# Kernel tuning notes

Hardware: AMD Instinct MI355X
Metric: run time of the kernel (lower is better)

The kernel has to match this reference:

```python
import jax, jax.numpy as jnp
import numpy as np

MOMENTUM = 0.05
EPS = 1e-06


def _gated_ema(x, g):
    """y[t] = (1 - g[t]) * y[t-1] + g[t] * x[t], y[-1] = 0.
    x: (B, C, T), g: (B, 1, T) -> (B, C, T)"""
    xT = jnp.moveaxis(x, -1, 0)  # (T, B, C)
    gT = jnp.moveaxis(g, -1, 0)  # (T, B, 1)
    init = jnp.zeros(x.shape[:-1], x.dtype)  # (B, C)

    def step(carry, inp):
        xt, gt = inp
        carry = (1.0 - gt) * carry + gt * xt
        return carry, carry

    _, ys = jax.lax.scan(step, init, (xT, gT))
    return jnp.moveaxis(ys, 0, -1)


def setup_inputs() -> dict:
    key = jax.random.key(0)
    ks = jax.random.split(key, 6)
    B, C, T = 8, 512, 8192
    return {
        "x": jax.random.normal(ks[0], (B, C, T), dtype=jnp.float32),
        "g": jax.random.uniform(ks[1], (B, 1, T), dtype=jnp.float32),
        "Wa_w": jax.random.normal(ks[2], (1, C, 1), dtype=jnp.float32),
        "Wb_w": jax.random.normal(ks[3], (1, C, 1), dtype=jnp.float32),
        "Wo_w": jax.random.normal(ks[4], (C, 1, 1), dtype=jnp.float32),
        "Wo_b": jax.random.normal(ks[5], (C,), dtype=jnp.float32),
    }


def reference(x, g, Wa_w, Wb_w, Wo_w, Wo_b):
    sg = jax.lax.stop_gradient
    C = x.shape[1]
    g = g * MOMENTUM  # time-varying momentum gate
    # Wa: 1x1 conv C->1 with softmax over input channels (convex combination)
    wa = jax.nn.softmax(Wa_w, axis=1)  # (1, C, 1)
    mean = jnp.sum(wa * _gated_ema(sg(x), g), axis=1, keepdims=True)  # (B, 1, T)
    xc = x - mean
    wb = jax.nn.softmax(Wb_w, axis=1)  # (1, C, 1)
    var = jnp.sum(wb * _gated_ema(jnp.square(sg(xc)), g), axis=1, keepdims=True)  # (B, 1, T)
    xn = xc / jnp.sqrt(var + EPS)
    # Wo: grouped 1x1 conv (groups=C) == per-channel scale + bias
    return xn * Wo_w.reshape(1, C, 1) + Wo_b.reshape(1, C, 1)
```

## Files before the change

kernel.cpp:

```cpp
#include <hip/hip_runtime.h>

constexpr int BB = 8, CC = 512, TT = 8192;
static_assert((TT & (TT - 1)) == 0 && (CC & (CC - 1)) == 0, "pow2");
constexpr int LOG_T = 13, LOG_C = 9;
constexpr float MOM = 0.05f, EPSV = 1e-6f;

typedef float v4f __attribute__((ext_vector_type(4)));

__global__ __launch_bounds__(256) void k_reduce_c(const float* __restrict__ x,
                                                  const float* __restrict__ Wa,
                                                  const float* __restrict__ Wb,
                                                  float* __restrict__ sa,
                                                  float* __restrict__ sb,
                                                  float* __restrict__ sb2) {
  __shared__ float lwa[CC];
  __shared__ float lwb[CC];
  __shared__ float xw[8];
  __shared__ float red[3][4][256];
  const int tid = threadIdx.x;
  const int lane = tid & 63;
  const int wid = tid >> 6;

  float va0 = Wa[tid], va1 = Wa[tid + 256];
  float vb0 = Wb[tid], vb1 = Wb[tid + 256];
  float ma = fmaxf(va0, va1), mb = fmaxf(vb0, vb1);
  #pragma unroll
  for (int off = 32; off > 0; off >>= 1) {
    ma = fmaxf(ma, __shfl_down(ma, off, 64));
    mb = fmaxf(mb, __shfl_down(mb, off, 64));
  }
  if (lane == 0) { xw[wid] = ma; xw[4 + wid] = mb; }
  __syncthreads();
  ma = fmaxf(fmaxf(xw[0], xw[1]), fmaxf(xw[2], xw[3]));
  mb = fmaxf(fmaxf(xw[4], xw[5]), fmaxf(xw[6], xw[7]));
  float ea0 = expf(va0 - ma), ea1 = expf(va1 - ma);
  float eb0 = expf(vb0 - mb), eb1 = expf(vb1 - mb);
  float sA = ea0 + ea1, sB = eb0 + eb1;
  #pragma unroll
  for (int off = 32; off > 0; off >>= 1) {
    sA += __shfl_down(sA, off, 64);
    sB += __shfl_down(sB, off, 64);
  }
  __syncthreads();
  if (lane == 0) { xw[wid] = sA; xw[4 + wid] = sB; }
  __syncthreads();
  sA = xw[0] + xw[1] + xw[2] + xw[3];
  sB = xw[4] + xw[5] + xw[6] + xw[7];
  const float rA = 1.f / sA, rB = 1.f / sB;
  lwa[tid] = ea0 * rA; lwa[tid + 256] = ea1 * rA;
  lwb[tid] = eb0 * rB; lwb[tid + 256] = eb1 * rB;
  __syncthreads();

  const int tilesPerB = TT / 256;
  const int b = blockIdx.x / tilesPerB;
  const int tbase = (blockIdx.x % tilesPerB) * 256;
  const int t = tbase + lane * 4;
  const float* xp = x + ((size_t)(b * CC + wid * 128)) * TT + t;

  float a0=0,a1=0,a2=0,a3=0;
  float b0=0,b1=0,b2=0,b3=0;
  float q0=0,q1=0,q2=0,q3=0;
  const int cbase = wid * 128;
  #pragma unroll 4
  for (int cc = 0; cc < 128; ++cc) {
    float4 xv = *(const float4*)(xp + (size_t)cc * TT);
    float wac = lwa[cbase + cc];
    float wbc = lwb[cbase + cc];
    a0 = fmaf(wac, xv.x, a0); a1 = fmaf(wac, xv.y, a1);
    a2 = fmaf(wac, xv.z, a2); a3 = fmaf(wac, xv.w, a3);
    b0 = fmaf(wbc, xv.x, b0); b1 = fmaf(wbc, xv.y, b1);
    b2 = fmaf(wbc, xv.z, b2); b3 = fmaf(wbc, xv.w, b3);
    q0 = fmaf(wbc * xv.x, xv.x, q0); q1 = fmaf(wbc * xv.y, xv.y, q1);
    q2 = fmaf(wbc * xv.z, xv.z, q2); q3 = fmaf(wbc * xv.w, xv.w, q3);
  }
  const int li = lane * 4;
  red[0][wid][li+0]=a0; red[0][wid][li+1]=a1; red[0][wid][li+2]=a2; red[0][wid][li+3]=a3;
  red[1][wid][li+0]=b0; red[1][wid][li+1]=b1; red[1][wid][li+2]=b2; red[1][wid][li+3]=b3;
  red[2][wid][li+0]=q0; red[2][wid][li+1]=q1; red[2][wid][li+2]=q2; red[2][wid][li+3]=q3;
  __syncthreads();

  if (tid < 64) {
    const int o = tid * 4;
    float oa[4], ob[4], oq[4];
    #pragma unroll
    for (int k = 0; k < 4; ++k) {
      oa[k] = red[0][0][o+k] + red[0][1][o+k] + red[0][2][o+k] + red[0][3][o+k];
      ob[k] = red[1][0][o+k] + red[1][1][o+k] + red[1][2][o+k] + red[1][3][o+k];
      oq[k] = red[2][0][o+k] + red[2][1][o+k] + red[2][2][o+k] + red[2][3][o+k];
    }
    const size_t dst = (size_t)b * TT + tbase + o;
    *(float4*)(sa  + dst) = make_float4(oa[0], oa[1], oa[2], oa[3]);
    *(float4*)(sb  + dst) = make_float4(ob[0], ob[1], ob[2], ob[3]);
    *(float4*)(sb2 + dst) = make_float4(oq[0], oq[1], oq[2], oq[3]);
  }
}

__device__ __forceinline__ float affine_scan_prev(float A, float B, int tid,
                                                  float* wAs, float* wBs) {
  const int lane = tid & 63;
  const int wid = tid >> 6;
  #pragma unroll
  for (int off = 1; off < 64; off <<= 1) {
    float pA = __shfl_up(A, off, 64);
    float pB = __shfl_up(B, off, 64);
    if (lane >= off) { B = fmaf(A, pB, B); A *= pA; }
  }
  __syncthreads();
  if (lane == 63) { wAs[wid] = A; wBs[wid] = B; }
  __syncthreads();
  float cB = 0.f;
  for (int w = 0; w < wid; ++w) cB = fmaf(wAs[w], cB, wBs[w]);
  float leA = __shfl_up(A, 1, 64);
  float leB = __shfl_up(B, 1, 64);
  if (lane == 0) { leA = 1.f; leB = 0.f; }
  return fmaf(leA, cB, leB);
}

__global__ __launch_bounds__(256) void k_scan(const float* __restrict__ g,
                                              const float* __restrict__ sa,
                                              const float* __restrict__ sb,
                                              const float* __restrict__ sb2,
                                              float* __restrict__ mean,
                                              float* __restrict__ inv) {
  constexpr int CH = TT / 256;
  __shared__ float wAs[4], wBs[4];
  const int tid = threadIdx.x;
  const size_t base = (size_t)blockIdx.x * TT + (size_t)tid * CH;

  float gt[CH], pa[CH];

  float A = 1.f, Bv = 0.f;
  #pragma unroll
  for (int j = 0; j < CH; j += 4) {
    float gv[4]; *(float4*)gv = *(const float4*)(g + base + j);
    float sv[4]; *(float4*)sv = *(const float4*)(sa + base + j);
    #pragma unroll
    for (int k = 0; k < 4; ++k) {
      float gg = gv[k] * MOM;
      gt[j + k] = gg;
      float p = gg * sv[k];
      pa[j + k] = p;
      float a = 1.f - gg;
      A *= a;
      Bv = fmaf(a, Bv, p);
    }
  }
  float m = affine_scan_prev(A, Bv, tid, wAs, wBs);

  float A2 = 1.f, B2 = 0.f;
  #pragma unroll
  for (int j = 0; j < CH; j += 4) {
    float bv[4]; *(float4*)bv = *(const float4*)(sb  + base + j);
    float qv[4]; *(float4*)qv = *(const float4*)(sb2 + base + j);
    float m4[4];
    #pragma unroll
    for (int k = 0; k < 4; ++k) {
      float a = 1.f - gt[j + k];
      m = fmaf(a, m, pa[j + k]);
      m4[k] = m;
      float vi = fmaf(m, m, fmaf(-2.f * m, bv[k], qv[k]));
      float pv = gt[j + k] * vi;
      pa[j + k] = pv;
      A2 *= a;
      B2 = fmaf(a, B2, pv);
    }
    *(float4*)(mean + base + j) = *(float4*)m4;
  }
  float v = affine_scan_prev(A2, B2, tid, wAs, wBs);

  #pragma unroll
  for (int j = 0; j < CH; j += 4) {
    float i4[4];
    #pragma unroll
    for (int k = 0; k < 4; ++k) {
      v = fmaf(1.f - gt[j + k], v, pa[j + k]);
      i4[k] = rsqrtf(v + EPSV);
    }
    *(float4*)(inv + base + j) = *(float4*)i4;
  }
}

__global__ __launch_bounds__(256) void k_out(const float* __restrict__ x,
                                             const float* __restrict__ mean,
                                             const float* __restrict__ inv,
                                             const float* __restrict__ wo,
                                             const float* __restrict__ bo,
                                             float* __restrict__ out) {
  const size_t n4 = (size_t)BB * CC * TT / 4;
  const size_t stride = (size_t)gridDim.x * blockDim.x;
  for (size_t i = (size_t)blockIdx.x * blockDim.x + threadIdx.x; i < n4; i += stride) {
    const size_t flat = i * 4;
    const int t = (int)(flat & (TT - 1));
    const size_t rem = flat >> LOG_T;
    const int c = (int)(rem & (CC - 1));
    const int b = (int)(rem >> LOG_C);
    float4 xv = *(const float4*)(x + flat);
    const size_t mi = ((size_t)b << LOG_T) + t;
    float4 m4 = *(const float4*)(mean + mi);
    float4 i4 = *(const float4*)(inv + mi);
    const float w = wo[c], bb = bo[c];
    v4f o;
    o.x = fmaf((xv.x - m4.x) * i4.x, w, bb);
    o.y = fmaf((xv.y - m4.y) * i4.y, w, bb);
    o.z = fmaf((xv.z - m4.z) * i4.z, w, bb);
    o.w = fmaf((xv.w - m4.w) * i4.w, w, bb);
    __builtin_nontemporal_store(o, (v4f*)(out + flat));
  }
}

extern "C" void kernel_launch(void* const* d_in, const int* in_sizes, int n_in,
                              void* d_out, int out_size, void* d_ws, size_t ws_size,
                              hipStream_t stream) {
  const float* x    = (const float*)d_in[0];
  const float* g    = (const float*)d_in[1];
  const float* Wa_w = (const float*)d_in[2];
  const float* Wb_w = (const float*)d_in[3];
  const float* Wo_w = (const float*)d_in[4];
  const float* Wo_b = (const float*)d_in[5];
  float* out = (float*)d_out;

  constexpr int BT = BB * TT;
  float* ws   = (float*)d_ws;
  float* sa   = ws;
  float* sb   = sa + BT;
  float* sb2  = sb + BT;
  float* mean = sb2 + BT;
  float* inv  = mean + BT;

  k_reduce_c<<<BB * (TT / 256), 256, 0, stream>>>(x, Wa_w, Wb_w, sa, sb, sb2);
  k_scan<<<BB, 256, 0, stream>>>(g, sa, sb, sb2, mean, inv);
  k_out<<<2048, 256, 0, stream>>>(x, mean, inv, Wo_w, Wo_b, out);
}
```

Baseline: 83.13 us.

## Widen blocks in reduce and scan kernels, unroll fixed-work output kernel

The channel-reduction kernel now uses 512 threads (8 waves, 64 channels each) to get more loads in flight per time tile. The scan kernel moves to 1024 threads with 8 elements per thread and preloads all inputs up front, which shortens the serial per-thread chain; the cross-wave prefix, however, is now a loop over 16 waves. The output kernel replaces its grid-stride loop with a fixed 4-iteration unrolled body over 8192 blocks. This adds more synchronisation overhead in the scan and uses more LDS in the reduction.

Result: no change. 82.52 us (-0.7%).

```diff
diff --git a/kernel.cpp b/kernel.cpp
--- a/kernel.cpp
+++ b/kernel.cpp
@@ -7,7 +7,7 @@
 
 typedef float v4f __attribute__((ext_vector_type(4)));
 
-__global__ __launch_bounds__(256) void k_reduce_c(const float* __restrict__ x,
+__global__ __launch_bounds__(512) void k_reduce_c(const float* __restrict__ x,
                                                   const float* __restrict__ Wa,
                                                   const float* __restrict__ Wb,
                                                   float* __restrict__ sa,
@@ -15,54 +15,52 @@
                                                   float* __restrict__ sb2) {
   __shared__ float lwa[CC];
   __shared__ float lwb[CC];
-  __shared__ float xw[8];
-  __shared__ float red[3][4][256];
+  __shared__ float xw[32];
+  __shared__ float red[3][8][256];
   const int tid = threadIdx.x;
   const int lane = tid & 63;
   const int wid = tid >> 6;
 
-  float va0 = Wa[tid], va1 = Wa[tid + 256];
-  float vb0 = Wb[tid], vb1 = Wb[tid + 256];
-  float ma = fmaxf(va0, va1), mb = fmaxf(vb0, vb1);
+  float va = Wa[tid], vb = Wb[tid];
+  float ma = va, mb = vb;
   #pragma unroll
   for (int off = 32; off > 0; off >>= 1) {
     ma = fmaxf(ma, __shfl_down(ma, off, 64));
     mb = fmaxf(mb, __shfl_down(mb, off, 64));
   }
-  if (lane == 0) { xw[wid] = ma; xw[4 + wid] = mb; }
-  __syncthreads();
-  ma = fmaxf(fmaxf(xw[0], xw[1]), fmaxf(xw[2], xw[3]));
-  mb = fmaxf(fmaxf(xw[4], xw[5]), fmaxf(xw[6], xw[7]));
-  float ea0 = expf(va0 - ma), ea1 = expf(va1 - ma);
-  float eb0 = expf(vb0 - mb), eb1 = expf(vb1 - mb);
-  float sA = ea0 + ea1, sB = eb0 + eb1;
+  if (lane == 0) { xw[wid] = ma; xw[8 + wid] = mb; }
+  __syncthreads();
+  ma = xw[0]; mb = xw[8];
+  #pragma unroll
+  for (int w = 1; w < 8; ++w) { ma = fmaxf(ma, xw[w]); mb = fmaxf(mb, xw[8 + w]); }
+  float ea = expf(va - ma), eb = expf(vb - mb);
+  float sA = ea, sB = eb;
   #pragma unroll
   for (int off = 32; off > 0; off >>= 1) {
     sA += __shfl_down(sA, off, 64);
     sB += __shfl_down(sB, off, 64);
   }
-  __syncthreads();
-  if (lane == 0) { xw[wid] = sA; xw[4 + wid] = sB; }
-  __syncthreads();
-  sA = xw[0] + xw[1] + xw[2] + xw[3];
-  sB = xw[4] + xw[5] + xw[6] + xw[7];
-  const float rA = 1.f / sA, rB = 1.f / sB;
-  lwa[tid] = ea0 * rA; lwa[tid + 256] = ea1 * rA;
-  lwb[tid] = eb0 * rB; lwb[tid + 256] = eb1 * rB;
+  if (lane == 0) { xw[16 + wid] = sA; xw[24 + wid] = sB; }
+  __syncthreads();
+  sA = xw[16]; sB = xw[24];
+  #pragma unroll
+  for (int w = 1; w < 8; ++w) { sA += xw[16 + w]; sB += xw[24 + w]; }
+  lwa[tid] = ea * (1.f / sA);
+  lwb[tid] = eb * (1.f / sB);
   __syncthreads();
 
   const int tilesPerB = TT / 256;
   const int b = blockIdx.x / tilesPerB;
   const int tbase = (blockIdx.x % tilesPerB) * 256;
   const int t = tbase + lane * 4;
-  const float* xp = x + ((size_t)(b * CC + wid * 128)) * TT + t;
+  const int cbase = wid * 64;
+  const float* xp = x + ((size_t)(b * CC + cbase)) * TT + t;
 
   float a0=0,a1=0,a2=0,a3=0;
   float b0=0,b1=0,b2=0,b3=0;
   float q0=0,q1=0,q2=0,q3=0;
-  const int cbase = wid * 128;
-  #pragma unroll 4
-  for (int cc = 0; cc < 128; ++cc) {
+  #pragma unroll 8
+  for (int cc = 0; cc < 64; ++cc) {
     float4 xv = *(const float4*)(xp + (size_t)cc * TT);
     float wac = lwa[cbase + cc];
     float wbc = lwb[cbase + cc];
@@ -81,12 +79,15 @@
 
   if (tid < 64) {
     const int o = tid * 4;
-    float oa[4], ob[4], oq[4];
+    float oa[4] = {0,0,0,0}, ob[4] = {0,0,0,0}, oq[4] = {0,0,0,0};
     #pragma unroll
-    for (int k = 0; k < 4; ++k) {
-      oa[k] = red[0][0][o+k] + red[0][1][o+k] + red[0][2][o+k] + red[0][3][o+k];
-      ob[k] = red[1][0][o+k] + red[1][1][o+k] + red[1][2][o+k] + red[1][3][o+k];
-      oq[k] = red[2][0][o+k] + red[2][1][o+k] + red[2][2][o+k] + red[2][3][o+k];
+    for (int w = 0; w < 8; ++w) {
+      #pragma unroll
+      for (int k = 0; k < 4; ++k) {
+        oa[k] += red[0][w][o+k];
+        ob[k] += red[1][w][o+k];
+        oq[k] += red[2][w][o+k];
+      }
     }
     const size_t dst = (size_t)b * TT + tbase + o;
     *(float4*)(sa  + dst) = make_float4(oa[0], oa[1], oa[2], oa[3]);
@@ -116,68 +117,67 @@
   return fmaf(leA, cB, leB);
 }
 
-__global__ __launch_bounds__(256) void k_scan(const float* __restrict__ g,
-                                              const float* __restrict__ sa,
-                                              const float* __restrict__ sb,
-                                              const float* __restrict__ sb2,
-                                              float* __restrict__ mean,
-                                              float* __restrict__ inv) {
-  constexpr int CH = TT / 256;
-  __shared__ float wAs[4], wBs[4];
+__global__ __launch_bounds__(1024) void k_scan(const float* __restrict__ g,
+                                               const float* __restrict__ sa,
+                                               const float* __restrict__ sb,
+                                               const float* __restrict__ sb2,
+                                               float* __restrict__ mean,
+                                               float* __restrict__ inv) {
+  constexpr int CH = 8;
+  __shared__ float wAs[16], wBs[16];
   const int tid = threadIdx.x;
   const size_t base = (size_t)blockIdx.x * TT + (size_t)tid * CH;
 
+  float gv[CH], av[CH], bv[CH], qv[CH];
+  *(float4*)(gv)     = *(const float4*)(g   + base);
+  *(float4*)(gv + 4) = *(const float4*)(g   + base + 4);
+  *(float4*)(av)     = *(const float4*)(sa  + base);
+  *(float4*)(av + 4) = *(const float4*)(sa  + base + 4);
+  *(float4*)(bv)     = *(const float4*)(sb  + base);
+  *(float4*)(bv + 4) = *(const float4*)(sb  + base + 4);
+  *(float4*)(qv)     = *(const float4*)(sb2 + base);
+  *(float4*)(qv + 4) = *(const float4*)(sb2 + base + 4);
+
   float gt[CH], pa[CH];
-
   float A = 1.f, Bv = 0.f;
   #pragma unroll
-  for (int j = 0; j < CH; j += 4) {
-    float gv[4]; *(float4*)gv = *(const float4*)(g + base + j);
-    float sv[4]; *(float4*)sv = *(const float4*)(sa + base + j);
-    #pragma unroll
-    for (int k = 0; k < 4; ++k) {
-      float gg = gv[k] * MOM;
-      gt[j + k] = gg;
-      float p = gg * sv[k];
-      pa[j + k] = p;
-      float a = 1.f - gg;
-      A *= a;
-      Bv = fmaf(a, Bv, p);
-    }
+  for (int j = 0; j < CH; ++j) {
+    float gg = gv[j] * MOM;
+    gt[j] = gg;
+    float p = gg * av[j];
+    pa[j] = p;
+    float a = 1.f - gg;
+    A *= a;
+    Bv = fmaf(a, Bv, p);
   }
   float m = affine_scan_prev(A, Bv, tid, wAs, wBs);
 
+  float m4[CH];
   float A2 = 1.f, B2 = 0.f;
   #pragma unroll
-  for (int j = 0; j < CH; j += 4) {
-    float bv[4]; *(float4*)bv = *(const float4*)(sb  + base + j);
-    float qv[4]; *(float4*)qv = *(const float4*)(sb2 + base + j);
-    float m4[4];
-    #pragma unroll
-    for (int k = 0; k < 4; ++k) {
-      float a = 1.f - gt[j + k];
-      m = fmaf(a, m, pa[j + k]);
-      m4[k] = m;
-      float vi = fmaf(m, m, fmaf(-2.f * m, bv[k], qv[k]));
-      float pv = gt[j + k] * vi;
-      pa[j + k] = pv;
-      A2 *= a;
-      B2 = fmaf(a, B2, pv);
-    }
-    *(float4*)(mean + base + j) = *(float4*)m4;
-  }
+  for (int j = 0; j < CH; ++j) {
+    float a = 1.f - gt[j];
+    m = fmaf(a, m, pa[j]);
+    m4[j] = m;
+    float vi = fmaf(m, m, fmaf(-2.f * m, bv[j], qv[j]));
+    float pv = gt[j] * vi;
+    pa[j] = pv;
+    A2 *= a;
+    B2 = fmaf(a, B2, pv);
+  }
+  *(float4*)(mean + base)     = *(float4*)(m4);
+  *(float4*)(mean + base + 4) = *(float4*)(m4 + 4);
+
   float v = affine_scan_prev(A2, B2, tid, wAs, wBs);
 
-  #pragma unroll
-  for (int j = 0; j < CH; j += 4) {
-    float i4[4];
-    #pragma unroll
-    for (int k = 0; k < 4; ++k) {
-      v = fmaf(1.f - gt[j + k], v, pa[j + k]);
-      i4[k] = rsqrtf(v + EPSV);
-    }
-    *(float4*)(inv + base + j) = *(float4*)i4;
-  }
+  float i4[CH];
+  #pragma unroll
+  for (int j = 0; j < CH; ++j) {
+    v = fmaf(1.f - gt[j], v, pa[j]);
+    i4[j] = rsqrtf(v + EPSV);
+  }
+  *(float4*)(inv + base)     = *(float4*)(i4);
+  *(float4*)(inv + base + 4) = *(float4*)(i4 + 4);
 }
 
 __global__ __launch_bounds__(256) void k_out(const float* __restrict__ x,
@@ -186,10 +186,11 @@
                                              const float* __restrict__ wo,
                                              const float* __restrict__ bo,
                                              float* __restrict__ out) {
-  const size_t n4 = (size_t)BB * CC * TT / 4;
-  const size_t stride = (size_t)gridDim.x * blockDim.x;
-  for (size_t i = (size_t)blockIdx.x * blockDim.x + threadIdx.x; i < n4; i += stride) {
-    const size_t flat = i * 4;
+  const size_t base4 = (size_t)blockIdx.x * 1024 + threadIdx.x;
+  #pragma unroll
+  for (int j = 0; j < 4; ++j) {
+    const size_t idx = base4 + (size_t)j * 256;
+    const size_t flat = idx * 4;
     const int t = (int)(flat & (TT - 1));
     const size_t rem = flat >> LOG_T;
     const int c = (int)(rem & (CC - 1));
@@ -227,7 +228,7 @@
   float* mean = sb2 + BT;
   float* inv  = mean + BT;
 
-  k_reduce_c<<<BB * (TT / 256), 256, 0, stream>>>(x, Wa_w, Wb_w, sa, sb, sb2);
-  k_scan<<<BB, 256, 0, stream>>>(g, sa, sb, sb2, mean, inv);
-  k_out<<<2048, 256, 0, stream>>>(x, mean, inv, Wo_w, Wo_b, out);
-}
+  k_reduce_c<<<BB * (TT / 256), 512, 0, stream>>>(x, Wa_w, Wb_w, sa, sb, sb2);
+  k_scan<<<BB, 1024, 0, stream>>>(g, sa, sb, sb2, mean, inv);
+  k_out<<<8192, 256, 0, stream>>>(x, mean, inv, Wo_w, Wo_b, out);
+}
```
